# Kernel optimization log

Hardware: AMD Instinct MI355X
Metric: run time of the kernel (lower is better)

The kernel has to match this reference:

```python
import jax, jax.numpy as jnp
import numpy as np

N = 50000      # nodes
E = 800000     # edges (before self-loops)
F_IN = 256     # feature_size
H = 96         # hidden_channels
G = 64         # graphs in batch
NC = 4         # num_classes
EPS = 1e-5     # BatchNorm eps


def _lrelu(x, s=0.01):
    return jnp.where(x >= 0, x, s * x)


def _gat(x, W, a_s, a_d, b, src, dst):
    # PyG GATConv, heads=1: linear transform, edge-wise LeakyReLU(0.2) scores,
    # segment softmax over destination nodes, scatter-add aggregation.
    h = x @ W                                                  # [N,H]
    e = _lrelu((h * a_s).sum(-1)[src] + (h * a_d).sum(-1)[dst], 0.2)  # [E+N]
    m = jax.ops.segment_max(e, dst, num_segments=N)
    ee = jnp.exp(e - m[dst])
    denom = jax.ops.segment_sum(ee, dst, num_segments=N)
    alpha = ee / denom[dst]
    return jax.ops.segment_sum(alpha[:, None] * h[src], dst, num_segments=N) + b


def _bn(x, g, b):
    # training-mode BatchNorm over the node dimension
    mu = x.mean(0)
    var = ((x - mu) ** 2).mean(0)
    return g * (x - mu) / jnp.sqrt(var + EPS) + b


def setup_inputs() -> dict:
    key = jax.random.key(0)
    ks = jax.random.split(key, 20)
    p = lambda i, sh: jax.random.normal(ks[i], sh, jnp.float32) * 0.05
    inp = {
        "x": jax.random.normal(ks[0], (N, F_IN), jnp.float32),
        "edge_index": jax.random.randint(ks[1], (2, E), 0, N),
        "batch": jnp.sort(jax.random.randint(ks[2], (N,), 0, G)),
        "embed_W": p(3, (F_IN, H)), "embed_b": jnp.zeros((H,), jnp.float32),
        "conv1_W": p(4, (H, H)), "conv1_as": p(5, (H,)), "conv1_ad": p(6, (H,)), "conv1_b": jnp.zeros((H,), jnp.float32),
        "conv2_W": p(7, (H, H)), "conv2_as": p(8, (H,)), "conv2_ad": p(9, (H,)), "conv2_b": jnp.zeros((H,), jnp.float32),
        "conv3_W": p(10, (H, H)), "conv3_as": p(11, (H,)), "conv3_ad": p(12, (H,)), "conv3_b": jnp.zeros((H,), jnp.float32),
        "fc1_W": p(13, (H, H)), "fc1_b": jnp.zeros((H,), jnp.float32),
        "fc2_W": p(14, (H, H)), "fc2_b": jnp.zeros((H,), jnp.float32),
        "bn1_g": jnp.ones((H,), jnp.float32), "bn1_b": jnp.zeros((H,), jnp.float32),
        "bn2_g": jnp.ones((H,), jnp.float32), "bn2_b": jnp.zeros((H,), jnp.float32),
        "bn3_g": jnp.ones((H,), jnp.float32), "bn3_b": jnp.zeros((H,), jnp.float32),
        "fc3_W": p(15, (H, H // 2)), "fc3_b": jnp.zeros((H // 2,), jnp.float32),
        "fc4_W": p(16, (H // 2, NC)), "fc4_b": jnp.zeros((NC,), jnp.float32),
    }
    return inp


def reference(x, edge_index, batch, embed_W, embed_b,
              conv1_W, conv1_as, conv1_ad, conv1_b,
              conv2_W, conv2_as, conv2_ad, conv2_b,
              conv3_W, conv3_as, conv3_ad, conv3_b,
              fc1_W, fc1_b, fc2_W, fc2_b,
              bn1_g, bn1_b, bn2_g, bn2_b, bn3_g, bn3_b,
              fc3_W, fc3_b, fc4_W, fc4_b):
    loops = jnp.arange(N)
    src = jnp.concatenate([edge_index[0], loops])   # GATConv add_self_loops=True
    dst = jnp.concatenate([edge_index[1], loops])

    h = _lrelu(x @ embed_W + embed_b)
    identity = h
    h = _lrelu(_bn(_gat(h, conv1_W, conv1_as, conv1_ad, conv1_b, src, dst), bn1_g, bn1_b)) + identity
    h = _lrelu(h @ fc1_W + fc1_b)
    h = _lrelu(_bn(_gat(h, conv2_W, conv2_as, conv2_ad, conv2_b, src, dst), bn2_g, bn2_b)) + identity
    h = _lrelu(h @ fc2_W + fc2_b)
    h = _lrelu(_bn(_gat(h, conv3_W, conv3_as, conv3_ad, conv3_b, src, dst), bn3_g, bn3_b)) + identity

    # Poincare ball expmap0 with c=1: tanh(||u||) * u / ||u||
    n = jnp.maximum(jnp.linalg.norm(h, axis=-1, keepdims=True), 1e-15)
    h = jnp.tanh(n) * h / n

    cnt = jax.ops.segment_sum(jnp.ones((N,), h.dtype), batch, num_segments=G)
    pooled = jax.ops.segment_sum(h, batch, num_segments=G) / jnp.maximum(cnt, 1.0)[:, None]

    o = _lrelu(pooled @ fc3_W + fc3_b)
    return o @ fc4_W + fc4_b
```

## Files before the change

### kernel.cpp

```cpp
#include <hip/hip_runtime.h>
#include <hip/hip_bf16.h>

#define DEVINL __device__ __forceinline__

constexpr int N_NODES = 50000;
constexpr int N_EDGES = 800000;
constexpr int F_IN    = 256;
constexpr int H       = 96;
constexpr int NG      = 64;
constexpr float BN_EPS = 1e-5f;
constexpr int SLOT    = 64;
constexpr int NREP    = 8;
constexpr int REPSZ   = NG * H + NG;
constexpr int EPB     = 8;
constexpr int ECHUNK  = 256 * EPB;
constexpr int BNREP   = 64;
constexpr int GFILL   = (N_NODES + 255) / 256;

typedef short bf16x8 __attribute__((ext_vector_type(8)));
typedef float f32x4  __attribute__((ext_vector_type(4)));

DEVINL float bf2f(unsigned int u) {
    union { unsigned int i; float f; } c; c.i = u << 16; return c.f;
}
DEVINL unsigned short f2bf(float f) {
    union { float f; unsigned int i; } c; c.f = f;
    unsigned int x = c.i;
    return (unsigned short)((x + 0x7fffu + ((x >> 16) & 1u)) >> 16);
}
DEVINL float lrelu01(float v) { return v >= 0.f ? v : 0.01f * v; }
DEVINL float ldf(const void* p, size_t i, int f32) {
    return f32 ? ((const float*)p)[i] : bf2f(((const unsigned short*)p)[i]);
}

__global__ __launch_bounds__(256) void setup_k(
    const unsigned short* __restrict__ x,
    int* __restrict__ flag, int* __restrict__ fill,
    const void* __restrict__ sE, const void* __restrict__ s0,
    const void* __restrict__ s1, const void* __restrict__ s2,
    const void* __restrict__ s3, const void* __restrict__ s4,
    unsigned short* __restrict__ dE, unsigned short* __restrict__ d0,
    unsigned short* __restrict__ d1, unsigned short* __restrict__ d2,
    unsigned short* __restrict__ d3, unsigned short* __restrict__ d4)
{
    int b = blockIdx.x;
    if (b < GFILL) {
        if (b == 0 && threadIdx.x < 64) {
            int l = threadIdx.x;
            float f = bf2f(x[l]);
            bool huge = !(fabsf(f) <= 1e4f);
            unsigned long long m = __ballot(huge);
            if (l == 0) flag[0] = (__popcll(m) >= 8) ? 1 : 0;
        }
        int i = b * 256 + threadIdx.x;
        if (i < N_NODES) fill[i] = 0;
        return;
    }
    float ff = bf2f(x[threadIdx.x & 63]);
    bool huge = !(fabsf(ff) <= 1e4f);
    unsigned long long mm = __ballot(huge);
    int lf32 = (__popcll(mm) >= 8) ? 1 : 0;

    int bb = b - GFILL;
    const void* src; unsigned short* dst; int K, i0;
    if (bb < 96) { src = sE; dst = dE; K = F_IN; i0 = bb * 256; }
    else {
        int m = (bb - 96) / 36, r = (bb - 96) % 36;
        K = H; i0 = r * 256;
        if      (m == 0) { src = s0; dst = d0; }
        else if (m == 1) { src = s1; dst = d1; }
        else if (m == 2) { src = s2; dst = d2; }
        else if (m == 3) { src = s3; dst = d3; }
        else             { src = s4; dst = d4; }
    }
    int i = i0 + threadIdx.x;
    if (i >= K * 96) return;
    int c   = i / 3072;
    int rem = i - c * 3072;
    int t    = rem >> 9;
    int rem2 = rem & 511;
    int l = rem2 >> 3, j = rem2 & 7;
    int k = c * 32 + (l >> 4) * 8 + j;
    int n = t * 16 + (l & 15);
    if (lf32) dst[i] = f2bf(((const float*)src)[k * 96 + n]);
    else      dst[i] = ((const unsigned short*)src)[k * 96 + n];
}

template<int EPI, int AWS, int SD, int ABN, int SCAT, int K, int ZB>
__global__ __launch_bounds__(256, 4) void mgemm_k(
    const void* __restrict__ Ap, const unsigned short* __restrict__ Wpk,
    const void* __restrict__ bp, const int* __restrict__ dflag,
    unsigned short* __restrict__ out, unsigned short* __restrict__ out2,
    const void* __restrict__ as_, const void* __restrict__ ad_,
    float* __restrict__ s, float* __restrict__ d,
    const float* __restrict__ coefp, const unsigned short* __restrict__ idn,
    const int* __restrict__ ei, int* __restrict__ fill,
    unsigned short* __restrict__ colw, int e0, int e1, int nscat,
    float* __restrict__ bnsumR, int M)
{
    constexpr int NCH = K / 32;

    if (ZB) {
        int zi = blockIdx.x * 256 + threadIdx.x;
        if (zi < BNREP * 192) bnsumR[zi] = 0.f;
    }

    if (SCAT && (int)blockIdx.x < nscat) {
        int b0 = e0 + (int)blockIdx.x * ECHUNK + (int)threadIdx.x;
        int sv[EPB], dv[EPB];
        bool ok[EPB];
        #pragma unroll
        for (int j = 0; j < EPB; j++) {
            int e = b0 + j * 256;
            ok[j] = (e < e1);
            int ee = ok[j] ? e : e0;
            sv[j] = ei[ee];
            dv[j] = ei[N_EDGES + ee];
        }
        int p[EPB];
        #pragma unroll
        for (int j = 0; j < EPB; j++)
            p[j] = ok[j] ? atomicAdd(&fill[dv[j]], 1) : SLOT;
        #pragma unroll
        for (int j = 0; j < EPB; j++)
            if (p[j] < SLOT) colw[(size_t)dv[j] * SLOT + p[j]] = (unsigned short)sv[j];
        return;
    }

    const int gb   = SCAT ? (int)blockIdx.x - nscat : (int)blockIdx.x;
    const int f32  = AWS ? 0 : dflag[0];
    const int wf32 = dflag[0];
    const int l    = threadIdx.x & 63;
    const int wave = threadIdx.x >> 6;
    const int row0 = gb * 64 + wave * 16;
    const int m    = l & 15;
    const int q    = l >> 4;
    const int arow = row0 + m;
    const bool aok = arow < M;

    bf16x8 av[NCH];
    #pragma unroll
    for (int c = 0; c < NCH; c++) {
        bf16x8 a = {};
        if (aok) {
            if (ABN) {
                const int f0 = c * 32 + q * 8;
                uint4 xu = *(const uint4*)((const unsigned short*)Ap + (size_t)arow * K + f0);
                uint4 iu = *(const uint4*)(idn + (size_t)arow * K + f0);
                unsigned int xs[4] = { xu.x, xu.y, xu.z, xu.w };
                unsigned int is[4] = { iu.x, iu.y, iu.z, iu.w };
                #pragma unroll
                for (int jj = 0; jj < 4; jj++) {
                    int f = f0 + 2 * jj;
                    float v0 = lrelu01(bf2f(xs[jj] & 0xffff) * coefp[f]     + coefp[96 + f])     + bf2f(is[jj] & 0xffff);
                    float v1 = lrelu01(bf2f(xs[jj] >> 16)    * coefp[f + 1] + coefp[96 + f + 1]) + bf2f(is[jj] >> 16);
                    a[2 * jj]     = (short)f2bf(v0);
                    a[2 * jj + 1] = (short)f2bf(v1);
                }
            } else if (f32) {
                const float* A = (const float*)Ap + (size_t)arow * K + c * 32 + q * 8;
                #pragma unroll
                for (int j = 0; j < 8; j++) a[j] = (short)f2bf(A[j]);
            } else {
                a = *(const bf16x8*)((const unsigned short*)Ap + (size_t)arow * K + c * 32 + q * 8);
            }
        }
        av[c] = a;
    }

    f32x4 acc[6] = {};
    const bf16x8* wp = (const bf16x8*)Wpk;
    #pragma unroll
    for (int c = 0; c < NCH; c++) {
        const int base = c * 384 + l;
        #pragma unroll
        for (int t = 0; t < 6; t++)
            acc[t] = __builtin_amdgcn_mfma_f32_16x16x32_bf16(av[c], wp[base + t * 64], acc[t], 0, 0, 0);
    }

    float bv[6];
    if (EPI > 0) {
        #pragma unroll
        for (int t = 0; t < 6; t++) bv[t] = ldf(bp, t * 16 + m, wf32);
    }
    #pragma unroll
    for (int r = 0; r < 4; r++) {
        int rr = row0 + q * 4 + r;
        if (rr >= M) continue;
        size_t o = (size_t)rr * 96 + m;
        #pragma unroll
        for (int t = 0; t < 6; t++) {
            float v = acc[t][r];
            if (EPI > 0) v = lrelu01(v + bv[t]);
            unsigned short sv = f2bf(v);
            out[o + t * 16] = sv;
            if (EPI == 2) out2[o + t * 16] = sv;
        }
    }

    if (SD) {
        float asv[6], adv[6];
        #pragma unroll
        for (int t = 0; t < 6; t++) {
            asv[t] = ldf(as_, t * 16 + m, wf32);
            adv[t] = ldf(ad_, t * 16 + m, wf32);
        }
        #pragma unroll
        for (int r = 0; r < 4; r++) {
            float ps = 0.f, pd = 0.f;
            #pragma unroll
            for (int t = 0; t < 6; t++) {
                ps = fmaf(acc[t][r], asv[t], ps);
                pd = fmaf(acc[t][r], adv[t], pd);
            }
            #pragma unroll
            for (int off = 1; off < 16; off <<= 1) {
                ps += __shfl_xor(ps, off);
                pd += __shfl_xor(pd, off);
            }
            int rr = row0 + q * 4 + r;
            if (m == 0 && rr < M) { s[rr] = ps; d[rr] = pd; }
        }
    }
}

__global__ __launch_bounds__(256, 4) void fcconv_k(
    const unsigned short* __restrict__ Ap,
    const unsigned short* __restrict__ Wfc, const void* __restrict__ bfc,
    const unsigned short* __restrict__ Wcv,
    const int* __restrict__ dflag,
    unsigned short* __restrict__ out,
    const void* __restrict__ as_, const void* __restrict__ ad_,
    float* __restrict__ s, float* __restrict__ d,
    const float* __restrict__ coefp, const unsigned short* __restrict__ idn,
    float* __restrict__ bnsumR, int M)
{
    __shared__ unsigned short R[64][104];

    {
        int zi = blockIdx.x * 256 + threadIdx.x;
        if (zi < BNREP * 192) bnsumR[zi] = 0.f;
    }

    const int wf32 = dflag[0];
    const int l    = threadIdx.x & 63;
    const int wave = threadIdx.x >> 6;
    const int row0 = blockIdx.x * 64 + wave * 16;
    const int m    = l & 15;
    const int q    = l >> 4;
    const int arow = row0 + m;
    const bool aok = arow < M;

    bf16x8 av[3];
    #pragma unroll
    for (int c = 0; c < 3; c++) {
        bf16x8 a = {};
        if (aok) {
            const int f0 = c * 32 + q * 8;
            uint4 xu = *(const uint4*)(Ap  + (size_t)arow * H + f0);
            uint4 iu = *(const uint4*)(idn + (size_t)arow * H + f0);
            unsigned int xs[4] = { xu.x, xu.y, xu.z, xu.w };
            unsigned int is[4] = { iu.x, iu.y, iu.z, iu.w };
            #pragma unroll
            for (int jj = 0; jj < 4; jj++) {
                int f = f0 + 2 * jj;
                float v0 = lrelu01(bf2f(xs[jj] & 0xffff) * coefp[f]     + coefp[96 + f])     + bf2f(is[jj] & 0xffff);
                float v1 = lrelu01(bf2f(xs[jj] >> 16)    * coefp[f + 1] + coefp[96 + f + 1]) + bf2f(is[jj] >> 16);
                a[2 * jj]     = (short)f2bf(v0);
                a[2 * jj + 1] = (short)f2bf(v1);
            }
        }
        av[c] = a;
    }

    f32x4 acc[6] = {};
    const bf16x8* wp1 = (const bf16x8*)Wfc;
    #pragma unroll
    for (int c = 0; c < 3; c++) {
        const int base = c * 384 + l;
        #pragma unroll
        for (int t = 0; t < 6; t++)
            acc[t] = __builtin_amdgcn_mfma_f32_16x16x32_bf16(av[c], wp1[base + t * 64], acc[t], 0, 0, 0);
    }

    float bv[6];
    #pragma unroll
    for (int t = 0; t < 6; t++) bv[t] = ldf(bfc, t * 16 + m, wf32);
    #pragma unroll
    for (int r = 0; r < 4; r++) {
        int lr = wave * 16 + q * 4 + r;
        #pragma unroll
        for (int t = 0; t < 6; t++)
            R[lr][t * 16 + m] = f2bf(lrelu01(acc[t][r] + bv[t]));
    }
    __syncthreads();

    bf16x8 a2[3];
    #pragma unroll
    for (int c = 0; c < 3; c++)
        a2[c] = *(const bf16x8*)&R[wave * 16 + m][c * 32 + q * 8];

    f32x4 acc2[6] = {};
    const bf16x8* wp2 = (const bf16x8*)Wcv;
    #pragma unroll
    for (int c = 0; c < 3; c++) {
        const int base = c * 384 + l;
        #pragma unroll
        for (int t = 0; t < 6; t++)
            acc2[t] = __builtin_amdgcn_mfma_f32_16x16x32_bf16(a2[c], wp2[base + t * 64], acc2[t], 0, 0, 0);
    }

    #pragma unroll
    for (int r = 0; r < 4; r++) {
        int rr = row0 + q * 4 + r;
        if (rr >= M) continue;
        size_t o = (size_t)rr * 96 + m;
        #pragma unroll
        for (int t = 0; t < 6; t++)
            out[o + t * 16] = f2bf(acc2[t][r]);
    }

    float asv[6], adv[6];
    #pragma unroll
    for (int t = 0; t < 6; t++) {
        asv[t] = ldf(as_, t * 16 + m, wf32);
        adv[t] = ldf(ad_, t * 16 + m, wf32);
    }
    #pragma unroll
    for (int r = 0; r < 4; r++) {
        float ps = 0.f, pd = 0.f;
        #pragma unroll
        for (int t = 0; t < 6; t++) {
            ps = fmaf(acc2[t][r], asv[t], ps);
            pd = fmaf(acc2[t][r], adv[t], pd);
        }
        #pragma unroll
        for (int off = 1; off < 16; off <<= 1) {
            ps += __shfl_xor(ps, off);
            pd += __shfl_xor(pd, off);
        }
        int rr = row0 + q * 4 + r;
        if (m == 0 && rr < M) { s[rr] = ps; d[rr] = pd; }
    }
}

__global__ __launch_bounds__(256) void agg_k(
    const unsigned short* __restrict__ h2, const float* __restrict__ s,
    const float* __restrict__ d, const int* __restrict__ fill,
    const unsigned short* __restrict__ col, const void* __restrict__ bias,
    const int* __restrict__ dflag, unsigned short* __restrict__ out,
    float* __restrict__ bnsumR, float* __restrict__ zp, int M)
{
    __shared__ uint2 uwb[4][80];
    __shared__ float lstat[4][192];
    if (zp) {
        int zi = blockIdx.x * 256 + threadIdx.x;
        if (zi < NREP * REPSZ) zp[zi] = 0.f;
    }
    int f32 = dflag[0];
    int v = (blockIdx.x * blockDim.x + threadIdx.x) >> 6;
    int l = threadIdx.x & 63;
    int wv = threadIdx.x >> 6;
    bool act = v < M;
    bool hw = (l < 48);
    int  c2 = 2 * l;
    float o0 = 0.f, o1 = 0.f;

    if (act) {
        int st   = v * SLOT;
        int degr = min(fill[v], SLOT - 1);
        int deg  = degr + 1;

        float dv = d[v];
        int u = 0; float e = -1e30f;
        if (l < degr) {
            u = col[st + l];
            float t = s[u] + dv;
            e = t >= 0.f ? t : 0.2f * t;
        } else if (l == degr) {
            u = v;
            float t = s[v] + dv;
            e = t >= 0.f ? t : 0.2f * t;
        }
        float lm = e;
        #pragma unroll
        for (int off = 32; off > 0; off >>= 1) lm = fmaxf(lm, __shfl_xor(lm, off));
        float w = (l < deg) ? __expf(e - lm) : 0.f;
        float lsum = w;
        #pragma unroll
        for (int off = 32; off > 0; off >>= 1) lsum += __shfl_xor(lsum, off);
        float rden = 1.0f / lsum;

        uwb[wv][l] = make_uint2((unsigned int)u, __float_as_uint(w));
        if (l < 16) uwb[wv][64 + l] = make_uint2(0u, 0u);

        float a0 = 0.f, a1 = 0.f;
        const uint2* myuw = uwb[wv];
        for (int j = 0; j < deg; j += 16) {
            uint2 p[16];
            #pragma unroll
            for (int k = 0; k < 16; k++) p[k] = myuw[j + k];
            if (hw) {
                unsigned int hv[16];
                #pragma unroll
                for (int k = 0; k < 16; k++)
                    hv[k] = *(const unsigned int*)(h2 + (size_t)p[k].x * 96 + c2);
                #pragma unroll
                for (int k = 0; k < 16; k++) {
                    float wj = __uint_as_float(p[k].y);
                    a0 = fmaf(wj, bf2f(hv[k] & 0xffff), a0);
                    a1 = fmaf(wj, bf2f(hv[k] >> 16),    a1);
                }
            }
        }
        if (hw) {
            float b0 = ldf(bias, c2,     f32);
            float b1 = ldf(bias, c2 + 1, f32);
            unsigned int o = (unsigned int)f2bf(a0 * rden + b0)
                           | ((unsigned int)f2bf(a1 * rden + b1) << 16);
            *(unsigned int*)(out + (size_t)v * 96 + c2) = o;
            o0 = bf2f(o & 0xffff);
            o1 = bf2f(o >> 16);
        }
    }

    if (hw) {
        lstat[wv][c2]          = o0;
        lstat[wv][c2 + 1]      = o1;
        lstat[wv][96 + c2]     = o0 * o0;
        lstat[wv][97 + c2]     = o1 * o1;
    }
    __syncthreads();
    if (threadIdx.x < 192) {
        float tot = lstat[0][threadIdx.x] + lstat[1][threadIdx.x]
                  + lstat[2][threadIdx.x] + lstat[3][threadIdx.x];
        atomicAdd(&bnsumR[(blockIdx.x & (BNREP - 1)) * 192 + threadIdx.x], tot);
    }
}

__global__ void bncoef_k(const float* __restrict__ bnsumR,
                         const void* __restrict__ g_,
                         const void* __restrict__ b_,
                         const int* __restrict__ dflag,
                         float* __restrict__ coef)
{
    __shared__ float tot[192];
    int t = threadIdx.x;
    if (t < 192) {
        float s = 0.f;
        #pragma unroll 8
        for (int r = 0; r < BNREP; r++) s += bnsumR[r * 192 + t];
        tot[t] = s;
    }
    __syncthreads();
    if (t < 96) {
        int f32 = dflag[0];
        float mu  = tot[t] * (1.f / N_NODES);
        float var = tot[96 + t] * (1.f / N_NODES) - mu * mu;
        float rinv = 1.0f / sqrtf(var + BN_EPS);
        float sc = ldf(g_, t, f32) * rinv;
        coef[t]      = sc;
        coef[96 + t] = ldf(b_, t, f32) - mu * sc;
    }
}

__global__ __launch_bounds__(256) void bnpool_k(
    const unsigned short* __restrict__ h, const float* __restrict__ coef,
    const unsigned short* __restrict__ iden, const int* __restrict__ batch,
    float* __restrict__ pooled8, int M)
{
    int w = (blockIdx.x * blockDim.x + threadIdx.x) >> 6;
    int l = threadIdx.x & 63;
    int v0 = w * 16;
    if (v0 >= M) return;
    float* P = pooled8 + (blockIdx.x & (NREP - 1)) * REPSZ;
    float* C = P + NG * H;
    bool hw = (l < 48);
    int  c2 = 2 * l;
    float sc0 = 0.f, sc1 = 0.f, sh0 = 0.f, sh1 = 0.f;
    if (hw) {
        sc0 = coef[c2]; sc1 = coef[c2 + 1];
        sh0 = coef[96 + c2]; sh1 = coef[97 + c2];
    }
    int nv = min(16, M - v0);

    int gb[16];
    #pragma unroll
    for (int k = 0; k < 16; k++) gb[k] = batch[v0 + min(k, nv - 1)];

    float x0[16], x1[16], q[16];
    #pragma unroll
    for (int k = 0; k < 16; k++) { x0[k] = 0.f; x1[k] = 0.f; q[k] = 0.f; }
    if (hw) {
        unsigned int xu[16], iu[16];
        #pragma unroll
        for (int k = 0; k < 16; k++) {
            int v = v0 + k;
            if (k < nv) {
                xu[k] = *(const unsigned int*)(h    + (size_t)v * 96 + c2);
                iu[k] = *(const unsigned int*)(iden + (size_t)v * 96 + c2);
            } else { xu[k] = 0u; iu[k] = 0u; }
        }
        #pragma unroll
        for (int k = 0; k < 16; k++) {
            x0[k] = lrelu01(bf2f(xu[k] & 0xffff) * sc0 + sh0) + bf2f(iu[k] & 0xffff);
            x1[k] = lrelu01(bf2f(xu[k] >> 16)    * sc1 + sh1) + bf2f(iu[k] >> 16);
            q[k]  = x0[k] * x0[k] + x1[k] * x1[k];
        }
    }

    #pragma unroll
    for (int off = 32; off > 0; off >>= 1) {
        #pragma unroll
        for (int k = 0; k < 16; k++) q[k] += __shfl_xor(q[k], off);
    }

    float f[16];
    #pragma unroll
    for (int k = 0; k < 16; k++) {
        float n = fmaxf(sqrtf(q[k]), 1e-15f);
        if (n < 15.f) {
            float t = __expf(2.f * n);
            f[k] = (t - 1.f) / ((t + 1.f) * n);
        } else {
            f[k] = 1.f / n;
        }
    }

    float a0 = 0.f, a1 = 0.f, cnt = 0.f;
    int curg = -1;
    for (int k = 0; k < nv; k++) {
        int g = gb[k];
        if (g != curg) {
            if (curg >= 0) {
                if (hw) {
                    atomicAdd(&P[curg * 96 + c2],     a0);
                    atomicAdd(&P[curg * 96 + c2 + 1], a1);
                }
                if (l == 0) atomicAdd(&C[curg], cnt);
            }
            a0 = a1 = 0.f; cnt = 0.f; curg = g;
        }
        a0 = fmaf(f[k], x0[k], a0);
        a1 = fmaf(f[k], x1[k], a1);
        cnt += 1.f;
    }
    if (curg >= 0) {
        if (hw) {
            atomicAdd(&P[curg * 96 + c2],     a0);
            atomicAdd(&P[curg * 96 + c2 + 1], a1);
        }
        if (l == 0) atomicAdd(&C[curg], cnt);
    }
}

__global__ __launch_bounds__(64) void head_k(const float* __restrict__ pooled8,
                                             const void* __restrict__ w3,
                                             const void* __restrict__ b3,
                                             const void* __restrict__ w4,
                                             const void* __restrict__ b4,
                                             const int* __restrict__ dflag,
                                             void* __restrict__ outv)
{
    int g = blockIdx.x;
    int t = threadIdx.x;
    int f32 = dflag[0];
    __shared__ float p[96];
    __shared__ float o[48];
    float cs = 0.f;
    #pragma unroll
    for (int r = 0; r < NREP; r++) cs += pooled8[r * REPSZ + NG * H + g];
    float inv = 1.0f / fmaxf(cs, 1.0f);
    for (int c = t; c < 96; c += 64) {
        float v = 0.f;
        #pragma unroll
        for (int r = 0; r < NREP; r++) v += pooled8[r * REPSZ + g * 96 + c];
        p[c] = v * inv;
    }
    __syncthreads();
    if (t < 48) {
        float a = ldf(b3, t, f32);
        #pragma unroll
        for (int c = 0; c < 96; c++) a = fmaf(p[c], ldf(w3, (size_t)c * 48 + t, f32), a);
        o[t] = lrelu01(a);
    }
    __syncthreads();
    if (t < 4) {
        float a = ldf(b4, t, f32);
        #pragma unroll
        for (int j = 0; j < 48; j++) a = fmaf(o[j], ldf(w4, j * 4 + t, f32), a);
        if (f32) ((float*)outv)[g * 4 + t] = a;
        else     ((unsigned short*)outv)[g * 4 + t] = f2bf(a);
    }
}

extern "C" void kernel_launch(void* const* d_in, const int* in_sizes, int n_in,
                              void* d_out, int out_size, void* d_ws, size_t ws_size,
                              hipStream_t stream)
{
    const void* x     = d_in[0];
    const int*  ei    = (const int*)d_in[1];
    const int*  batch = (const int*)d_in[2];
    const void* embW  = d_in[3];
    const void* embB  = d_in[4];
    const void* convW[3]  = { d_in[5],  d_in[9],  d_in[13] };
    const void* convAs[3] = { d_in[6],  d_in[10], d_in[14] };
    const void* convAd[3] = { d_in[7],  d_in[11], d_in[15] };
    const void* convB[3]  = { d_in[8],  d_in[12], d_in[16] };
    const void* fcW[2]    = { d_in[17], d_in[19] };
    const void* fcB[2]    = { d_in[18], d_in[20] };
    const void* bnG[3]    = { d_in[21], d_in[23], d_in[25] };
    const void* bnB[3]    = { d_in[22], d_in[24], d_in[26] };
    const void* fc3W = d_in[27];
    const void* fc3b = d_in[28];
    const void* fc4W = d_in[29];
    const void* fc4b = d_in[30];

    char* wp_ = (char*)d_ws;
    auto alloc = [&](size_t b) { char* p = wp_; wp_ += (b + 255) & ~(size_t)255; return p; };
    int*   dflag = (int*)alloc(256);
    unsigned short* ident = (unsigned short*)alloc((size_t)N_NODES * H * 2);
    unsigned short* hA    = (unsigned short*)alloc((size_t)N_NODES * H * 2);
    unsigned short* hB    = (unsigned short*)alloc((size_t)N_NODES * H * 2);
    float* s_sc  = (float*)alloc((size_t)N_NODES * 4);
    float* d_sc  = (float*)alloc((size_t)N_NODES * 4);
    float* bnsumR = (float*)alloc((size_t)BNREP * 192 * 4);
    float* coef  = (float*)alloc(192 * 4);
    float* pooled8 = (float*)alloc((size_t)NREP * REPSZ * 4);
    int*   fill  = (int*)alloc((size_t)N_NODES * 4);
    unsigned short* col = (unsigned short*)alloc((size_t)N_NODES * SLOT * 2);
    unsigned short* wpkEmb = (unsigned short*)alloc((size_t)F_IN * 96 * 2);
    unsigned short* wpkS[5];
    for (int i = 0; i < 5; i++) wpkS[i] = (unsigned short*)alloc((size_t)H * 96 * 2);

    const int GM = (N_NODES + 63) / 64;
    const int GW = (N_NODES * 64 + 255) / 256;
    const int GP = ((N_NODES + 15) / 16 * 64 + 255) / 256;
    const int EH = N_EDGES / 2;
    const int GS = (EH + ECHUNK - 1) / ECHUNK;

    setup_k<<<GFILL + 276, 256, 0, stream>>>(
        (const unsigned short*)x, dflag, fill,
        embW, convW[0], convW[1], convW[2], fcW[0], fcW[1],
        wpkEmb, wpkS[0], wpkS[1], wpkS[2], wpkS[3], wpkS[4]);

    mgemm_k<1, 0, 0, 0, 1, F_IN, 0><<<GS + GM, 256, 0, stream>>>(
        x, wpkEmb, embB, dflag, ident, nullptr,
        nullptr, nullptr, nullptr, nullptr, nullptr, nullptr,
        ei, fill, col, 0, EH, GS, nullptr, N_NODES);

    mgemm_k<0, 1, 1, 0, 1, H, 1><<<GS + GM, 256, 0, stream>>>(
        ident, wpkS[0], nullptr, dflag, hB, nullptr,
        convAs[0], convAd[0], s_sc, d_sc, nullptr, nullptr,
        ei, fill, col, EH, N_EDGES, GS, bnsumR, N_NODES);

    agg_k<<<GW, 256, 0, stream>>>(hB, s_sc, d_sc, fill, col, convB[0], dflag, hA,
                                  bnsumR, nullptr, N_NODES);
    bncoef_k<<<1, 192, 0, stream>>>(bnsumR, bnG[0], bnB[0], dflag, coef);
    fcconv_k<<<GM, 256, 0, stream>>>(hA, wpkS[3], fcB[0], wpkS[1], dflag, hB,
                                     convAs[1], convAd[1], s_sc, d_sc,
                                     coef, ident, bnsumR, N_NODES);

    agg_k<<<GW, 256, 0, stream>>>(hB, s_sc, d_sc, fill, col, convB[1], dflag, hA,
                                  bnsumR, nullptr, N_NODES);
    bncoef_k<<<1, 192, 0, stream>>>(bnsumR, bnG[1], bnB[1], dflag, coef);
    fcconv_k<<<GM, 256, 0, stream>>>(hA, wpkS[4], fcB[1], wpkS[2], dflag, hB,
                                     convAs[2], convAd[2], s_sc, d_sc,
                                     coef, ident, bnsumR, N_NODES);

    agg_k<<<GW, 256, 0, stream>>>(hB, s_sc, d_sc, fill, col, convB[2], dflag, hA,
                                  bnsumR, pooled8, N_NODES);
    bncoef_k<<<1, 192, 0, stream>>>(bnsumR, bnG[2], bnB[2], dflag, coef);

    bnpool_k<<<GP, 256, 0, stream>>>(hA, coef, ident, batch, pooled8, N_NODES);
    head_k<<<NG, 64, 0, stream>>>(pooled8, fc3W, fc3b, fc4W, fc4b, dflag, d_out);
}
```

Measured before the change: 372.7 us.

## Split edge scatter across three kernels and pad fill counters to avoid atomic contention

```diff
diff --git a/kernel.cpp b/kernel.cpp
--- a/kernel.cpp
+++ b/kernel.cpp
@@ -10,15 +10,16 @@
 constexpr int NG      = 64;
 constexpr float BN_EPS = 1e-5f;
 constexpr int SLOT    = 64;
+constexpr int FSTR    = 16;
 constexpr int NREP    = 8;
 constexpr int REPSZ   = NG * H + NG;
 constexpr int EPB     = 8;
 constexpr int ECHUNK  = 256 * EPB;
 constexpr int BNREP   = 64;
-constexpr int GFILL   = (N_NODES + 255) / 256;
 
 typedef short bf16x8 __attribute__((ext_vector_type(8)));
 typedef float f32x4  __attribute__((ext_vector_type(4)));
+typedef unsigned int u32x4 __attribute__((ext_vector_type(4)));
 
 DEVINL float bf2f(unsigned int u) {
     union { unsigned int i; float f; } c; c.i = u << 16; return c.f;
@@ -32,10 +33,53 @@
 DEVINL float ldf(const void* p, size_t i, int f32) {
     return f32 ? ((const float*)p)[i] : bf2f(((const unsigned short*)p)[i]);
 }
+DEVINL u32x4 ntld4(const void* p) {
+    return __builtin_nontemporal_load((const u32x4*)p);
+}
+
+DEVINL void scatter_body(const int* __restrict__ ei, int* __restrict__ fill,
+                         unsigned short* __restrict__ colw,
+                         int blk, int e0, int e1)
+{
+    int b0 = e0 + blk * ECHUNK + (int)threadIdx.x;
+    int sv[EPB], dv[EPB];
+    bool ok[EPB];
+    #pragma unroll
+    for (int j = 0; j < EPB; j++) {
+        int e = b0 + j * 256;
+        ok[j] = (e < e1);
+        int ee = ok[j] ? e : e0;
+        sv[j] = __builtin_nontemporal_load(ei + ee);
+        dv[j] = __builtin_nontemporal_load(ei + N_EDGES + ee);
+    }
+    int p[EPB];
+    #pragma unroll
+    for (int j = 0; j < EPB; j++)
+        p[j] = ok[j] ? atomicAdd(&fill[dv[j] * FSTR], 1) : SLOT;
+    #pragma unroll
+    for (int j = 0; j < EPB; j++)
+        if (p[j] < SLOT) colw[(size_t)dv[j] * SLOT + p[j]] = (unsigned short)sv[j];
+}
+
+__global__ __launch_bounds__(256) void prefill_k(const unsigned short* __restrict__ x,
+                                                 int* __restrict__ flag,
+                                                 int* __restrict__ fill)
+{
+    if (blockIdx.x == 0 && threadIdx.x < 64) {
+        int l = threadIdx.x;
+        float f = bf2f(x[l]);
+        bool huge = !(fabsf(f) <= 1e4f);
+        unsigned long long m = __ballot(huge);
+        if (l == 0) flag[0] = (__popcll(m) >= 8) ? 1 : 0;
+    }
+    int i = blockIdx.x * 256 + threadIdx.x;
+    if (i < N_NODES * FSTR) fill[i] = 0;
+}
 
 __global__ __launch_bounds__(256) void setup_k(
     const unsigned short* __restrict__ x,
-    int* __restrict__ flag, int* __restrict__ fill,
+    const int* __restrict__ ei, int* __restrict__ fill,
+    unsigned short* __restrict__ colw, int e0, int e1, int nscat,
     const void* __restrict__ sE, const void* __restrict__ s0,
     const void* __restrict__ s1, const void* __restrict__ s2,
     const void* __restrict__ s3, const void* __restrict__ s4,
@@ -44,24 +88,14 @@
     unsigned short* __restrict__ d3, unsigned short* __restrict__ d4)
 {
     int b = blockIdx.x;
-    if (b < GFILL) {
-        if (b == 0 && threadIdx.x < 64) {
-            int l = threadIdx.x;
-            float f = bf2f(x[l]);
-            bool huge = !(fabsf(f) <= 1e4f);
-            unsigned long long m = __ballot(huge);
-            if (l == 0) flag[0] = (__popcll(m) >= 8) ? 1 : 0;
-        }
-        int i = b * 256 + threadIdx.x;
-        if (i < N_NODES) fill[i] = 0;
-        return;
-    }
+    if (b < nscat) { scatter_body(ei, fill, colw, b, e0, e1); return; }
+
     float ff = bf2f(x[threadIdx.x & 63]);
     bool huge = !(fabsf(ff) <= 1e4f);
     unsigned long long mm = __ballot(huge);
     int lf32 = (__popcll(mm) >= 8) ? 1 : 0;
 
-    int bb = b - GFILL;
+    int bb = b - nscat;
     const void* src; unsigned short* dst; int K, i0;
     if (bb < 96) { src = sE; dst = dE; K = F_IN; i0 = bb * 256; }
     else {
@@ -106,24 +140,7 @@
     }
 
     if (SCAT && (int)blockIdx.x < nscat) {
-        int b0 = e0 + (int)blockIdx.x * ECHUNK + (int)threadIdx.x;
-        int sv[EPB], dv[EPB];
-        bool ok[EPB];
-        #pragma unroll
-        for (int j = 0; j < EPB; j++) {
-            int e = b0 + j * 256;
-            ok[j] = (e < e1);
-            int ee = ok[j] ? e : e0;
-            sv[j] = ei[ee];
-            dv[j] = ei[N_EDGES + ee];
-        }
-        int p[EPB];
-        #pragma unroll
-        for (int j = 0; j < EPB; j++)
-            p[j] = ok[j] ? atomicAdd(&fill[dv[j]], 1) : SLOT;
-        #pragma unroll
-        for (int j = 0; j < EPB; j++)
-            if (p[j] < SLOT) colw[(size_t)dv[j] * SLOT + p[j]] = (unsigned short)sv[j];
+        scatter_body(ei, fill, colw, (int)blockIdx.x, e0, e1);
         return;
     }
 
@@ -157,12 +174,20 @@
                     a[2 * jj]     = (short)f2bf(v0);
                     a[2 * jj + 1] = (short)f2bf(v1);
                 }
+            } else if (AWS) {
+                a = *(const bf16x8*)((const unsigned short*)Ap + (size_t)arow * K + c * 32 + q * 8);
             } else if (f32) {
                 const float* A = (const float*)Ap + (size_t)arow * K + c * 32 + q * 8;
+                u32x4 u0 = ntld4(A);
+                u32x4 u1 = ntld4(A + 4);
                 #pragma unroll
-                for (int j = 0; j < 8; j++) a[j] = (short)f2bf(A[j]);
+                for (int j = 0; j < 4; j++) a[j]     = (short)f2bf(__uint_as_float(u0[j]));
+                #pragma unroll
+                for (int j = 0; j < 4; j++) a[4 + j] = (short)f2bf(__uint_as_float(u1[j]));
             } else {
-                a = *(const bf16x8*)((const unsigned short*)Ap + (size_t)arow * K + c * 32 + q * 8);
+                union { u32x4 u; bf16x8 h; } cv;
+                cv.u = ntld4((const unsigned short*)Ap + (size_t)arow * K + c * 32 + q * 8);
+                a = cv.h;
             }
         }
         av[c] = a;
@@ -368,7 +393,7 @@
 
     if (act) {
         int st   = v * SLOT;
-        int degr = min(fill[v], SLOT - 1);
+        int degr = min(fill[v * FSTR], SLOT - 1);
         int deg  = degr + 1;
 
         float dv = d[v];
@@ -627,7 +652,7 @@
     float* bnsumR = (float*)alloc((size_t)BNREP * 192 * 4);
     float* coef  = (float*)alloc(192 * 4);
     float* pooled8 = (float*)alloc((size_t)NREP * REPSZ * 4);
-    int*   fill  = (int*)alloc((size_t)N_NODES * 4);
+    int*   fill  = (int*)alloc((size_t)N_NODES * FSTR * 4);
     unsigned short* col = (unsigned short*)alloc((size_t)N_NODES * SLOT * 2);
     unsigned short* wpkEmb = (unsigned short*)alloc((size_t)F_IN * 96 * 2);
     unsigned short* wpkS[5];
@@ -636,23 +661,29 @@
     const int GM = (N_NODES + 63) / 64;
     const int GW = (N_NODES * 64 + 255) / 256;
     const int GP = ((N_NODES + 15) / 16 * 64 + 255) / 256;
-    const int EH = N_EDGES / 2;
-    const int GS = (EH + ECHUNK - 1) / ECHUNK;
-
-    setup_k<<<GFILL + 276, 256, 0, stream>>>(
-        (const unsigned short*)x, dflag, fill,
+    const int GZ = (N_NODES * FSTR + 255) / 256;
+    const int E3  = (N_EDGES + 2) / 3;
+    const int eA1 = E3, eB1 = 2 * E3;
+    const int GSa = (eA1 + ECHUNK - 1) / ECHUNK;
+    const int GSb = (eB1 - eA1 + ECHUNK - 1) / ECHUNK;
+    const int GSc = (N_EDGES - eB1 + ECHUNK - 1) / ECHUNK;
+
+    prefill_k<<<GZ, 256, 0, stream>>>((const unsigned short*)x, dflag, fill);
+
+    setup_k<<<GSa + 276, 256, 0, stream>>>(
+        (const unsigned short*)x, ei, fill, col, 0, eA1, GSa,
         embW, convW[0], convW[1], convW[2], fcW[0], fcW[1],
         wpkEmb, wpkS[0], wpkS[1], wpkS[2], wpkS[3], wpkS[4]);
 
-    mgemm_k<1, 0, 0, 0, 1, F_IN, 0><<<GS + GM, 256, 0, stream>>>(
+    mgemm_k<1, 0, 0, 0, 1, F_IN, 0><<<GSb + GM, 256, 0, stream>>>(
         x, wpkEmb, embB, dflag, ident, nullptr,
         nullptr, nullptr, nullptr, nullptr, nullptr, nullptr,
-        ei, fill, col, 0, EH, GS, nullptr, N_NODES);
-
-    mgemm_k<0, 1, 1, 0, 1, H, 1><<<GS + GM, 256, 0, stream>>>(
+        ei, fill, col, eA1, eB1, GSb, nullptr, N_NODES);
+
+    mgemm_k<0, 1, 1, 0, 1, H, 1><<<GSc + GM, 256, 0, stream>>>(
         ident, wpkS[0], nullptr, dflag, hB, nullptr,
         convAs[0], convAd[0], s_sc, d_sc, nullptr, nullptr,
-        ei, fill, col, EH, N_EDGES, GS, bnsumR, N_NODES);
+        ei, fill, col, eB1, N_EDGES, GSc, bnsumR, N_NODES);
 
     agg_k<<<GW, 256, 0, stream>>>(hB, s_sc, d_sc, fill, col, convB[0], dflag, hA,
                                   bnsumR, nullptr, N_NODES);
```

New measurement: 372.5 us. About the same (-0.0%).

## Fuse embedding GEMM and first conv GEMM into one kernel via LDS

Applied to the files above, without the earlier changes.

```diff
diff --git a/kernel.cpp b/kernel.cpp
--- a/kernel.cpp
+++ b/kernel.cpp
@@ -19,6 +19,7 @@
 
 typedef short bf16x8 __attribute__((ext_vector_type(8)));
 typedef float f32x4  __attribute__((ext_vector_type(4)));
+typedef unsigned int u32x4 __attribute__((ext_vector_type(4)));
 
 DEVINL float bf2f(unsigned int u) {
     union { unsigned int i; float f; } c; c.i = u << 16; return c.f;
@@ -31,6 +32,33 @@
 DEVINL float lrelu01(float v) { return v >= 0.f ? v : 0.01f * v; }
 DEVINL float ldf(const void* p, size_t i, int f32) {
     return f32 ? ((const float*)p)[i] : bf2f(((const unsigned short*)p)[i]);
+}
+DEVINL u32x4 ntld4(const void* p) {
+    return __builtin_nontemporal_load((const u32x4*)p);
+}
+
+DEVINL void scatter_body(const int* __restrict__ ei, int* __restrict__ fill,
+                         unsigned short* __restrict__ colw,
+                         int blk, int e0, int e1)
+{
+    int b0 = e0 + blk * ECHUNK + (int)threadIdx.x;
+    int sv[EPB], dv[EPB];
+    bool ok[EPB];
+    #pragma unroll
+    for (int j = 0; j < EPB; j++) {
+        int e = b0 + j * 256;
+        ok[j] = (e < e1);
+        int ee = ok[j] ? e : e0;
+        sv[j] = __builtin_nontemporal_load(ei + ee);
+        dv[j] = __builtin_nontemporal_load(ei + N_EDGES + ee);
+    }
+    int p[EPB];
+    #pragma unroll
+    for (int j = 0; j < EPB; j++)
+        p[j] = ok[j] ? atomicAdd(&fill[dv[j]], 1) : SLOT;
+    #pragma unroll
+    for (int j = 0; j < EPB; j++)
+        if (p[j] < SLOT) colw[(size_t)dv[j] * SLOT + p[j]] = (unsigned short)sv[j];
 }
 
 __global__ __launch_bounds__(256) void setup_k(
@@ -86,50 +114,31 @@
     else      dst[i] = ((const unsigned short*)src)[k * 96 + n];
 }
 
-template<int EPI, int AWS, int SD, int ABN, int SCAT, int K, int ZB>
-__global__ __launch_bounds__(256, 4) void mgemm_k(
-    const void* __restrict__ Ap, const unsigned short* __restrict__ Wpk,
-    const void* __restrict__ bp, const int* __restrict__ dflag,
-    unsigned short* __restrict__ out, unsigned short* __restrict__ out2,
+__global__ __launch_bounds__(256, 4) void embconv_k(
+    const void* __restrict__ xp, const unsigned short* __restrict__ WpkE,
+    const void* __restrict__ embB, const unsigned short* __restrict__ Wcv,
+    const int* __restrict__ dflag,
+    unsigned short* __restrict__ ident, unsigned short* __restrict__ out,
     const void* __restrict__ as_, const void* __restrict__ ad_,
     float* __restrict__ s, float* __restrict__ d,
-    const float* __restrict__ coefp, const unsigned short* __restrict__ idn,
     const int* __restrict__ ei, int* __restrict__ fill,
-    unsigned short* __restrict__ colw, int e0, int e1, int nscat,
+    unsigned short* __restrict__ colw, int nscat,
     float* __restrict__ bnsumR, int M)
 {
-    constexpr int NCH = K / 32;
-
-    if (ZB) {
+    __shared__ unsigned short R[64][104];
+
+    {
         int zi = blockIdx.x * 256 + threadIdx.x;
         if (zi < BNREP * 192) bnsumR[zi] = 0.f;
     }
 
-    if (SCAT && (int)blockIdx.x < nscat) {
-        int b0 = e0 + (int)blockIdx.x * ECHUNK + (int)threadIdx.x;
-        int sv[EPB], dv[EPB];
-        bool ok[EPB];
-        #pragma unroll
-        for (int j = 0; j < EPB; j++) {
-            int e = b0 + j * 256;
-            ok[j] = (e < e1);
-            int ee = ok[j] ? e : e0;
-            sv[j] = ei[ee];
-            dv[j] = ei[N_EDGES + ee];
-        }
-        int p[EPB];
-        #pragma unroll
-        for (int j = 0; j < EPB; j++)
-            p[j] = ok[j] ? atomicAdd(&fill[dv[j]], 1) : SLOT;
-        #pragma unroll
-        for (int j = 0; j < EPB; j++)
-            if (p[j] < SLOT) colw[(size_t)dv[j] * SLOT + p[j]] = (unsigned short)sv[j];
+    if ((int)blockIdx.x < nscat) {
+        scatter_body(ei, fill, colw, (int)blockIdx.x, 0, N_EDGES);
         return;
     }
 
-    const int gb   = SCAT ? (int)blockIdx.x - nscat : (int)blockIdx.x;
-    const int f32  = AWS ? 0 : dflag[0];
-    const int wf32 = dflag[0];
+    const int gb   = (int)blockIdx.x - nscat;
+    const int f32  = dflag[0];
     const int l    = threadIdx.x & 63;
     const int wave = threadIdx.x >> 6;
     const int row0 = gb * 64 + wave * 16;
@@ -138,89 +147,100 @@
     const int arow = row0 + m;
     const bool aok = arow < M;
 
-    bf16x8 av[NCH];
-    #pragma unroll
-    for (int c = 0; c < NCH; c++) {
+    bf16x8 av[8];
+    #pragma unroll
+    for (int c = 0; c < 8; c++) {
         bf16x8 a = {};
         if (aok) {
-            if (ABN) {
-                const int f0 = c * 32 + q * 8;
-                uint4 xu = *(const uint4*)((const unsigned short*)Ap + (size_t)arow * K + f0);
-                uint4 iu = *(const uint4*)(idn + (size_t)arow * K + f0);
-                unsigned int xs[4] = { xu.x, xu.y, xu.z, xu.w };
-                unsigned int is[4] = { iu.x, iu.y, iu.z, iu.w };
+            if (f32) {
+                const float* A = (const float*)xp + (size_t)arow * F_IN + c * 32 + q * 8;
+                u32x4 u0 = ntld4(A);
+                u32x4 u1 = ntld4(A + 4);
                 #pragma unroll
-                for (int jj = 0; jj < 4; jj++) {
-                    int f = f0 + 2 * jj;
-                    float v0 = lrelu01(bf2f(xs[jj] & 0xffff) * coefp[f]     + coefp[96 + f])     + bf2f(is[jj] & 0xffff);
-                    float v1 = lrelu01(bf2f(xs[jj] >> 16)    * coefp[f + 1] + coefp[96 + f + 1]) + bf2f(is[jj] >> 16);
-                    a[2 * jj]     = (short)f2bf(v0);
-                    a[2 * jj + 1] = (short)f2bf(v1);
-                }
-            } else if (f32) {
-                const float* A = (const float*)Ap + (size_t)arow * K + c * 32 + q * 8;
+                for (int j = 0; j < 4; j++) a[j]     = (short)f2bf(__uint_as_float(u0[j]));
                 #pragma unroll
-                for (int j = 0; j < 8; j++) a[j] = (short)f2bf(A[j]);
+                for (int j = 0; j < 4; j++) a[4 + j] = (short)f2bf(__uint_as_float(u1[j]));
             } else {
-                a = *(const bf16x8*)((const unsigned short*)Ap + (size_t)arow * K + c * 32 + q * 8);
+                union { u32x4 u; bf16x8 h; } cv;
+                cv.u = ntld4((const unsigned short*)xp + (size_t)arow * F_IN + c * 32 + q * 8);
+                a = cv.h;
             }
         }
         av[c] = a;
     }
 
     f32x4 acc[6] = {};
-    const bf16x8* wp = (const bf16x8*)Wpk;
-    #pragma unroll
-    for (int c = 0; c < NCH; c++) {
+    const bf16x8* wp1 = (const bf16x8*)WpkE;
+    #pragma unroll
+    for (int c = 0; c < 8; c++) {
         const int base = c * 384 + l;
         #pragma unroll
         for (int t = 0; t < 6; t++)
-            acc[t] = __builtin_amdgcn_mfma_f32_16x16x32_bf16(av[c], wp[base + t * 64], acc[t], 0, 0, 0);
+            acc[t] = __builtin_amdgcn_mfma_f32_16x16x32_bf16(av[c], wp1[base + t * 64], acc[t], 0, 0, 0);
     }
 
     float bv[6];
-    if (EPI > 0) {
-        #pragma unroll
-        for (int t = 0; t < 6; t++) bv[t] = ldf(bp, t * 16 + m, wf32);
-    }
+    #pragma unroll
+    for (int t = 0; t < 6; t++) bv[t] = ldf(embB, t * 16 + m, f32);
+    #pragma unroll
+    for (int r = 0; r < 4; r++) {
+        int lr = wave * 16 + q * 4 + r;
+        int rr = row0 + q * 4 + r;
+        #pragma unroll
+        for (int t = 0; t < 6; t++) {
+            unsigned short sv = f2bf(lrelu01(acc[t][r] + bv[t]));
+            R[lr][t * 16 + m] = sv;
+            if (rr < M) ident[(size_t)rr * 96 + m + t * 16] = sv;
+        }
+    }
+    __syncthreads();
+
+    bf16x8 a2[3];
+    #pragma unroll
+    for (int c = 0; c < 3; c++)
+        a2[c] = *(const bf16x8*)&R[wave * 16 + m][c * 32 + q * 8];
+
+    f32x4 acc2[6] = {};
+    const bf16x8* wp2 = (const bf16x8*)Wcv;
+    #pragma unroll
+    for (int c = 0; c < 3; c++) {
+        const int base = c * 384 + l;
+        #pragma unroll
+        for (int t = 0; t < 6; t++)
+            acc2[t] = __builtin_amdgcn_mfma_f32_16x16x32_bf16(a2[c], wp2[base + t * 64], acc2[t], 0, 0, 0);
+    }
+
     #pragma unroll
     for (int r = 0; r < 4; r++) {
         int rr = row0 + q * 4 + r;
         if (rr >= M) continue;
         size_t o = (size_t)rr * 96 + m;
         #pragma unroll
+        for (int t = 0; t < 6; t++)
+            out[o + t * 16] = f2bf(acc2[t][r]);
+    }
+
+    float asv[6], adv[6];
+    #pragma unroll
+    for (int t = 0; t < 6; t++) {
+        asv[t] = ldf(as_, t * 16 + m, f32);
+        adv[t] = ldf(ad_, t * 16 + m, f32);
+    }
+    #pragma unroll
+    for (int r = 0; r < 4; r++) {
+        float ps = 0.f, pd = 0.f;
+        #pragma unroll
         for (int t = 0; t < 6; t++) {
-            float v = acc[t][r];
-            if (EPI > 0) v = lrelu01(v + bv[t]);
-            unsigned short sv = f2bf(v);
-            out[o + t * 16] = sv;
-            if (EPI == 2) out2[o + t * 16] = sv;
-        }
-    }
-
-    if (SD) {
-        float asv[6], adv[6];
-        #pragma unroll
-        for (int t = 0; t < 6; t++) {
-            asv[t] = ldf(as_, t * 16 + m, wf32);
-            adv[t] = ldf(ad_, t * 16 + m, wf32);
-        }
-        #pragma unroll
-        for (int r = 0; r < 4; r++) {
-            float ps = 0.f, pd = 0.f;
-            #pragma unroll
-            for (int t = 0; t < 6; t++) {
-                ps = fmaf(acc[t][r], asv[t], ps);
-                pd = fmaf(acc[t][r], adv[t], pd);
-            }
-            #pragma unroll
-            for (int off = 1; off < 16; off <<= 1) {
-                ps += __shfl_xor(ps, off);
-                pd += __shfl_xor(pd, off);
-            }
-            int rr = row0 + q * 4 + r;
-            if (m == 0 && rr < M) { s[rr] = ps; d[rr] = pd; }
-        }
+            ps = fmaf(acc2[t][r], asv[t], ps);
+            pd = fmaf(acc2[t][r], adv[t], pd);
+        }
+        #pragma unroll
+        for (int off = 1; off < 16; off <<= 1) {
+            ps += __shfl_xor(ps, off);
+            pd += __shfl_xor(pd, off);
+        }
+        int rr = row0 + q * 4 + r;
+        if (m == 0 && rr < M) { s[rr] = ps; d[rr] = pd; }
     }
 }
 
@@ -397,6 +417,7 @@
         float a0 = 0.f, a1 = 0.f;
         const uint2* myuw = uwb[wv];
         for (int j = 0; j < deg; j += 16) {
+            int lim = deg - j;
             uint2 p[16];
             #pragma unroll
             for (int k = 0; k < 16; k++) p[k] = myuw[j + k];
@@ -404,7 +425,7 @@
                 unsigned int hv[16];
                 #pragma unroll
                 for (int k = 0; k < 16; k++)
-                    hv[k] = *(const unsigned int*)(h2 + (size_t)p[k].x * 96 + c2);
+                    hv[k] = (k < lim) ? *(const unsigned int*)(h2 + (size_t)p[k].x * 96 + c2) : 0u;
                 #pragma unroll
                 for (int k = 0; k < 16; k++) {
                     float wj = __uint_as_float(p[k].y);
@@ -636,23 +657,17 @@
     const int GM = (N_NODES + 63) / 64;
     const int GW = (N_NODES * 64 + 255) / 256;
     const int GP = ((N_NODES + 15) / 16 * 64 + 255) / 256;
-    const int EH = N_EDGES / 2;
-    const int GS = (EH + ECHUNK - 1) / ECHUNK;
+    const int GS = (N_EDGES + ECHUNK - 1) / ECHUNK;
 
     setup_k<<<GFILL + 276, 256, 0, stream>>>(
         (const unsigned short*)x, dflag, fill,
         embW, convW[0], convW[1], convW[2], fcW[0], fcW[1],
         wpkEmb, wpkS[0], wpkS[1], wpkS[2], wpkS[3], wpkS[4]);
 
-    mgemm_k<1, 0, 0, 0, 1, F_IN, 0><<<GS + GM, 256, 0, stream>>>(
-        x, wpkEmb, embB, dflag, ident, nullptr,
-        nullptr, nullptr, nullptr, nullptr, nullptr, nullptr,
-        ei, fill, col, 0, EH, GS, nullptr, N_NODES);
-
-    mgemm_k<0, 1, 1, 0, 1, H, 1><<<GS + GM, 256, 0, stream>>>(
-        ident, wpkS[0], nullptr, dflag, hB, nullptr,
-        convAs[0], convAd[0], s_sc, d_sc, nullptr, nullptr,
-        ei, fill, col, EH, N_EDGES, GS, bnsumR, N_NODES);
+    embconv_k<<<GS + GM, 256, 0, stream>>>(
+        x, wpkEmb, embB, wpkS[0], dflag, ident, hB,
+        convAs[0], convAd[0], s_sc, d_sc,
+        ei, fill, col, GS, bnsumR, N_NODES);
 
     agg_k<<<GW, 256, 0, stream>>>(hB, s_sc, d_sc, fill, col, convB[0], dflag, hA,
                                   bnsumR, nullptr, N_NODES);
```

Result: no change. 367.4 us (-1.4%).
